# Performance work log

Hardware: AMD Instinct MI355X
Metric: run time of the kernel (lower is better)

The kernel has to match this reference:

```python
import jax, jax.numpy as jnp
import numpy as np

B, T, D, K = 4, 2048, 1024, 4

def setup_inputs() -> dict:
    key = jax.random.key(0)
    ks = jax.random.split(key, 4)
    u = jax.random.normal(ks[0], (B, T, D), dtype=jnp.float32)
    s0 = jnp.zeros((B, K, D), dtype=jnp.float32)
    W_in = jax.random.normal(ks[1], (K * D, D), dtype=jnp.float32) * (1.0 / np.sqrt(D))
    b_in = jnp.zeros((K * D,), dtype=jnp.float32)
    W_out = jax.random.normal(ks[2], (D, K * D), dtype=jnp.float32) * (1.0 / np.sqrt(K * D))
    b_out = jnp.zeros((D,), dtype=jnp.float32)
    decay_logit = jax.random.normal(ks[3], (K,), dtype=jnp.float32)
    return {"u": u, "s0": s0, "W_in": W_in, "b_in": b_in,
            "W_out": W_out, "b_out": b_out, "decay_logit": decay_logit}

def reference(u, s0, W_in, b_in, W_out, b_out, decay_logit):
    # u: (B,T,D); s0: (B,K,D)
    Bb, Tt, Dd = u.shape
    Kk = decay_logit.shape[0]
    # input projection -> (B,T,K,D) -> (T,B,K,D) for scan over time
    inp = (jnp.einsum('btd,ed->bte', u, W_in) + b_in).reshape(Bb, Tt, Kk, Dd)
    xs = jnp.transpose(inp, (1, 0, 2, 3))  # (T,B,K,D)
    decay = jax.nn.sigmoid(decay_logit).reshape(1, Kk, 1)  # (1,K,1)

    def step(s, x):
        s_next = decay * s + x
        return s_next, s_next

    s_last, s_seq = jax.lax.scan(step, s0, xs)  # s_seq: (T,B,K,D)
    g_in = jnp.transpose(s_seq, (1, 0, 2, 3)).reshape(Bb, Tt, Kk * Dd)
    g = jnp.einsum('bte,de->btd', g_in, W_out) + b_out
    return g, s_last
```

## Files before the change

kernel.cpp:

```cpp
#include <hip/hip_runtime.h>


#define Bb 4
#define Tt 2048
#define Dd 1024
#define Kk 4
#define BT (Bb*Tt)
#define Ee (Kk*Dd)
#define NCH 32
#define LCH 64

typedef __bf16 bf16x8 __attribute__((ext_vector_type(8)));
typedef float  f32x4  __attribute__((ext_vector_type(4)));

__device__ __forceinline__ float bf2f(ushort u){
  union { unsigned int i; float f; } x; x.i = ((unsigned int)u) << 16; return x.f;
}
__device__ __forceinline__ ushort f2bf(float f){
  union { unsigned int i; float f; } x; x.f = f;
  unsigned int i = x.i;
  return (ushort)((i + 0x7FFFu + ((i >> 16) & 1u)) >> 16);
}
__device__ __forceinline__ float lo16(unsigned u){
  union { unsigned i; float f; } x; x.i = u << 16; return x.f;
}
__device__ __forceinline__ float hi16(unsigned u){
  union { unsigned i; float f; } x; x.i = u & 0xFFFF0000u; return x.f;
}
__device__ __forceinline__ float sigm(float x){ return 1.0f / (1.0f + expf(-x)); }

__global__ __launch_bounds__(256) void k_f2bf4(const float4* __restrict__ in,
                                               ushort4* __restrict__ out, int n4){
  int i = blockIdx.x * 256 + threadIdx.x;
  if (i < n4){
    float4 v = in[i];
    ushort4 o; o.x = f2bf(v.x); o.y = f2bf(v.y); o.z = f2bf(v.z); o.w = f2bf(v.w);
    out[i] = o;
  }
}

__global__ __launch_bounds__(256) void k_transpose(const float* __restrict__ in,
                                                   ushort* __restrict__ out){
  __shared__ float tile[32][33];
  int tx = threadIdx.x, ty = threadIdx.y;
  int c0 = blockIdx.x * 32, r0 = blockIdx.y * 32;
  #pragma unroll
  for (int j = 0; j < 4; ++j)
    tile[ty + j*8][tx] = in[(size_t)(r0 + ty + j*8) * Dd + c0 + tx];
  __syncthreads();
  #pragma unroll
  for (int j = 0; j < 4; ++j)
    out[(size_t)(c0 + ty + j*8) * Ee + r0 + tx] = f2bf(tile[tx][ty + j*8]);
}

__global__ __launch_bounds__(256) void gemm_nt(const ushort* __restrict__ A,
                                               const ushort* __restrict__ B,
                                               ushort* __restrict__ C,
                                               int Kred, int lda, int ldb, int ldc,
                                               long aBatch, long bBatch, long cBatch){
  __shared__ ushort As[128 * 32];
  __shared__ ushort Bs[128 * 32];
  A += (long)blockIdx.z * aBatch;
  B += (long)blockIdx.z * bBatch;
  C += (long)blockIdx.z * cBatch;
  const int tid  = threadIdx.x;
  const int lane = tid & 63;
  const int w    = tid >> 6;
  const int wr   = w >> 1, wc = w & 1;
  const int rowBase = blockIdx.x * 128;
  const int colBase = blockIdx.y * 128;

  f32x4 acc[4][4] = {};
  const int krow = (lane >> 4) * 8;
  const int rsel = lane & 15;

  for (int kk = 0; kk < Kred; kk += 32){
    __syncthreads();
    #pragma unroll
    for (int i = 0; i < 2; ++i){
      int c  = i * 256 + tid;
      int r  = c >> 2;
      int c8 = (c & 3) * 8;
      const ushort* ga = A + (size_t)(rowBase + r) * lda + kk + c8;
      const ushort* gb = B + (size_t)(colBase + r) * ldb + kk + c8;
      __builtin_amdgcn_global_load_lds((const __attribute__((address_space(1))) void*)ga,
                                       (__attribute__((address_space(3))) void*)&As[c * 8],
                                       16, 0, 0);
      __builtin_amdgcn_global_load_lds((const __attribute__((address_space(1))) void*)gb,
                                       (__attribute__((address_space(3))) void*)&Bs[c * 8],
                                       16, 0, 0);
    }
    asm volatile("s_waitcnt vmcnt(0)" ::: "memory");
    __syncthreads();

    bf16x8 Af[4], Bf[4];
    #pragma unroll
    for (int mi = 0; mi < 4; ++mi)
      Af[mi] = *(const bf16x8*)&As[(wr*64 + mi*16 + rsel) * 32 + krow];
    #pragma unroll
    for (int ni = 0; ni < 4; ++ni)
      Bf[ni] = *(const bf16x8*)&Bs[(wc*64 + ni*16 + rsel) * 32 + krow];
    #pragma unroll
    for (int mi = 0; mi < 4; ++mi)
      #pragma unroll
      for (int ni = 0; ni < 4; ++ni)
        acc[mi][ni] = __builtin_amdgcn_mfma_f32_16x16x32_bf16(Af[mi], Bf[ni], acc[mi][ni], 0, 0, 0);
  }

  #pragma unroll
  for (int mi = 0; mi < 4; ++mi){
    #pragma unroll
    for (int ni = 0; ni < 4; ++ni){
      int r0 = rowBase + wr*64 + mi*16 + (lane >> 4) * 4;
      int c0 = colBase + wc*64 + ni*16 + (lane & 15);
      #pragma unroll
      for (int q = 0; q < 4; ++q)
        C[(size_t)(r0 + q) * ldc + c0] = f2bf(acc[mi][ni][q]);
    }
  }
}

#define STAGE_OP(GB, LOFF)                                                     \
  { _Pragma("unroll")                                                          \
    for (int i_ = 0; i_ < 2; ++i_){                                            \
      int c_ = tid + i_*256;                                                   \
      int row_ = c_ >> 2;                                                      \
      int ss_ = (c_ & 3) ^ ((row_ >> 2) & 3);                                  \
      const ushort* g_ = (GB) + (size_t)row_ * 1024 + ss_ * 8;                 \
      __builtin_amdgcn_global_load_lds(                                        \
        (const __attribute__((address_space(1))) void*)g_,                     \
        (__attribute__((address_space(3))) void*)&lds[(LOFF) + c_*8],          \
        16, 0, 0);                                                             \
    } }

#define LOAD_A4(DST)                                                           \
  { _Pragma("unroll")                                                          \
    for (int mi_ = 0; mi_ < 4; ++mi_){                                         \
      int r_ = wm*64 + mi_*16 + rsel;                                          \
      int uo_ = r_*32 + kq*8;                                                  \
      uo_ ^= ((uo_ >> 7) & 3) << 3;                                            \
      DST[mi_] = *(const bf16x8*)&lds[cbase + uo_];                            \
    } }

#define LOAD_B4(DST)                                                           \
  { _Pragma("unroll")                                                          \
    for (int ni_ = 0; ni_ < 4; ++ni_){                                         \
      int r_ = wn*64 + ni_*16 + rsel;                                          \
      int uo_ = r_*32 + kq*8;                                                  \
      uo_ ^= ((uo_ >> 7) & 3) << 3;                                            \
      DST[ni_] = *(const bf16x8*)&lds[cbase + 4096 + uo_];                     \
    } }

#define XB(R) ((((R) & 3) ^ (((R) >> 2) & 3)) << 5)
#define BAR() __builtin_amdgcn_s_barrier()

__global__ __launch_bounds__(256, 4) void gemm_big(const ushort* __restrict__ A,
                                                   const ushort* __restrict__ B,
                                                   ushort* __restrict__ C,
                                                   const float* __restrict__ dlog,
                                                   float* __restrict__ carry){
  __shared__ ushort lds[16384];
  const int tid  = threadIdx.x;
  const int lane = tid & 63;
  const int w    = tid >> 6;
  const int wm   = w >> 1;
  const int wn   = w & 1;
  const int rsel = lane & 15;
  const int kq   = lane >> 4;

  int bid = blockIdx.x;
  int xcd = bid & 7, rr = bid >> 3;
  const int rowBase = ((xcd >> 1) * 16 + (rr & 15)) * 128;
  const int colBase = ((xcd & 1) * 16 + (rr >> 4)) * 128;

  const ushort* Ag = A + (size_t)rowBase * 1024;
  const ushort* Bg = B + (size_t)colBase * 1024;

  f32x4 acc[4][4] = {};

  STAGE_OP(Ag +  0, 0);
  STAGE_OP(Bg +  0, 4096);
  STAGE_OP(Ag + 32, 8192);
  STAGE_OP(Bg + 32, 8192 + 4096);
  asm volatile("s_waitcnt vmcnt(4)" ::: "memory");
  BAR();

  for (int t = 0; t < 32; ++t){
    const int cbase = (t & 1) * 8192;
    bf16x8 af[4], bf[4];
    LOAD_A4(af); LOAD_B4(bf);
    #pragma unroll
    for (int mi = 0; mi < 4; ++mi)
      #pragma unroll
      for (int ni = 0; ni < 4; ++ni)
        acc[mi][ni] = __builtin_amdgcn_mfma_f32_16x16x32_bf16(af[mi], bf[ni], acc[mi][ni], 0, 0, 0);
    asm volatile("s_waitcnt lgkmcnt(0)" ::: "memory");
    BAR();
    if (t < 30){
      STAGE_OP(Ag + (t+2)*32, cbase);
      STAGE_OP(Bg + (t+2)*32, cbase + 4096);
      asm volatile("s_waitcnt vmcnt(4)" ::: "memory");
    } else {
      asm volatile("s_waitcnt vmcnt(0)" ::: "memory");
    }
    BAR();
  }

  #pragma unroll
  for (int mi = 0; mi < 4; ++mi){
    #pragma unroll
    for (int j = 0; j < 4; ++j){
      #pragma unroll
      for (int q = 0; q < 4; ++q){
        int row = wm*64 + mi*16 + (lane >> 4)*4 + q;
        int col = wn*64 + j*16 + rsel;
        int byte = (row*256 + col*2) ^ XB(row);
        *(ushort*)((char*)lds + byte) = f2bf(acc[mi][j][q]);
      }
    }
  }
  __syncthreads();

  if (tid < 128){
    const int k_blk = colBase >> 10;
    const int b_blk = rowBase >> 11;
    const int ch0   = (rowBase & 2047) >> 6;
    const int d0    = colBase & 1023;
    const float p   = sigm(dlog[k_blk]);
    int cp = tid & 63, ch = tid >> 6;
    float a0 = 0.f, a1 = 0.f;
    for (int i = 0; i < 64; ++i){
      int row = ch*64 + i;
      int byte = (row*256 + cp*4) ^ XB(row);
      unsigned v = *(const unsigned*)((char*)lds + byte);
      a0 = p * a0 + lo16(v);
      a1 = p * a1 + hi16(v);
    }
    float* cdst = &carry[(size_t)((b_blk*Kk + k_blk)*NCH + ch0 + ch) * Dd + d0 + cp*2];
    cdst[0] = a0; cdst[1] = a1;
  }

  #pragma unroll
  for (int j = 0; j < 8; ++j){
    int idx = tid + j*256;
    int r = idx >> 4, c16 = idx & 15;
    int byte = (r*256 + c16*16) ^ XB(r);
    f32x4 v = *(const f32x4*)((char*)lds + byte);
    *(f32x4*)&C[(size_t)(rowBase + r) * Ee + colBase + c16*8] = v;
  }
}

__global__ __launch_bounds__(256) void k_z0(const ushort* __restrict__ Wout_bf,
                                            const float* __restrict__ s0,
                                            float* __restrict__ z0){
  int gid  = blockIdx.x * 4 + (threadIdx.x >> 6);
  int lane = threadIdx.x & 63;
  int d = gid & 1023, k = (gid >> 10) & 3, b = gid >> 12;
  const ushort* wrow = Wout_bf + (size_t)d * Ee + k * Dd;
  const float* sv   = s0 + ((size_t)(b*Kk + k) << 10);
  float s = 0.f;
  #pragma unroll
  for (int j = 0; j < 2; ++j){
    int base = lane*8 + j*512;
    uint4 wv = *(const uint4*)(wrow + base);
    float4 sa = *(const float4*)(sv + base);
    float4 sb = *(const float4*)(sv + base + 4);
    s += lo16(wv.x)*sa.x + hi16(wv.x)*sa.y + lo16(wv.y)*sa.z + hi16(wv.y)*sa.w
       + lo16(wv.z)*sb.x + hi16(wv.z)*sb.y + lo16(wv.w)*sb.z + hi16(wv.w)*sb.w;
  }
  for (int off = 32; off; off >>= 1) s += __shfl_down(s, off);
  if (lane == 0) z0[gid] = s;
}

__global__ __launch_bounds__(256) void k_cterm(const ushort* __restrict__ Wout_bf,
                                               const float* __restrict__ b_in,
                                               float* __restrict__ cterm){
  int gid  = blockIdx.x * 4 + (threadIdx.x >> 6);
  int lane = threadIdx.x & 63;
  int d = gid & 1023, k = gid >> 10;
  const ushort* wrow = Wout_bf + (size_t)d * Ee + k * Dd;
  const float* bv   = b_in + k * Dd;
  float s = 0.f;
  #pragma unroll
  for (int j = 0; j < 2; ++j){
    int base = lane*8 + j*512;
    uint4 wv = *(const uint4*)(wrow + base);
    float4 sa = *(const float4*)(bv + base);
    float4 sb = *(const float4*)(bv + base + 4);
    s += lo16(wv.x)*sa.x + hi16(wv.x)*sa.y + lo16(wv.y)*sa.z + hi16(wv.y)*sa.w
       + lo16(wv.z)*sb.x + hi16(wv.z)*sb.y + lo16(wv.w)*sb.z + hi16(wv.w)*sb.w;
  }
  for (int off = 32; off; off >>= 1) s += __shfl_down(s, off);
  if (lane == 0) cterm[gid] = s;
}

__global__ __launch_bounds__(256) void k_scanInc(const float* __restrict__ carry,
                                                 const float* __restrict__ z0,
                                                 const float* __restrict__ dlog,
                                                 float* __restrict__ incoming){
  int idx = blockIdx.x * 256 + threadIdx.x;
  int k = (idx >> 10) & 3;
  int bk = idx >> 10, d = idx & 1023;
  float p  = sigm(dlog[k]);
  float dL = powf(p, (float)LCH);
  float inc = z0[idx];
  for (int c = 0; c < NCH; ++c){
    size_t o = ((size_t)(bk * NCH + c)) * Dd + d;
    incoming[o] = inc;
    inc = dL * inc + carry[o];
  }
}

__global__ __launch_bounds__(256) void k_scanB(const ushort* __restrict__ Y,
                                               const float* __restrict__ incoming,
                                               const float* __restrict__ dlog,
                                               const float* __restrict__ b_out,
                                               const float* __restrict__ cterm,
                                               float* __restrict__ g){
  int x = blockIdx.x;
  int d = blockIdx.y * 256 + threadIdx.x;
  int c = x & 31, b = x >> 5;
  float p[4], z[4], ct[4], pw[4];
  #pragma unroll
  for (int k = 0; k < 4; ++k){
    p[k]  = sigm(dlog[k]);
    z[k]  = incoming[((size_t)(((b*Kk + k))*NCH + c)) * Dd + d];
    float omp = fmaxf(1.0f - p[k], 1e-30f);
    ct[k] = cterm[k * Dd + d] / omp;
    pw[k] = powf(p[k], (float)(c * LCH + 1));
  }
  float bo = b_out[d];
  size_t ybase = ((size_t)(b*Tt + c*LCH)) * Ee + d;
  size_t gbase = ((size_t)(b*Tt + c*LCH)) * Dd + d;
  for (int i = 0; i < LCH; ++i){
    float acc = bo;
    #pragma unroll
    for (int k = 0; k < 4; ++k){
      z[k] = p[k] * z[k] + bf2f(Y[ybase + (size_t)k * Dd]);
      acc += z[k] + ct[k] * (1.0f - pw[k]);
      pw[k] *= p[k];
    }
    g[gbase] = acc;
    ybase += Ee; gbase += Dd;
  }
}

__global__ __launch_bounds__(256) void k_prep(const float* __restrict__ u,
                                              const float* __restrict__ dlog,
                                              float* __restrict__ vpart,
                                              ushort* __restrict__ U_bf){
  int x = blockIdx.x;
  int d = blockIdx.y * 256 + threadIdx.x;
  int c = x & 31, b = x >> 5;
  float p[4], a[4] = {0.f, 0.f, 0.f, 0.f};
  #pragma unroll
  for (int k = 0; k < 4; ++k) p[k] = sigm(dlog[k]);
  size_t ub = ((size_t)(b*Tt + c*LCH)) * Dd + d;
  for (int i = 0; i < LCH; ++i){
    float uv = u[ub];
    U_bf[ub] = f2bf(uv);
    #pragma unroll
    for (int k = 0; k < 4; ++k) a[k] = p[k] * a[k] + uv;
    ub += Dd;
  }
  #pragma unroll
  for (int k = 0; k < 4; ++k)
    vpart[(((size_t)x) * Kk + k) * Dd + d] = a[k];
}

__global__ __launch_bounds__(256) void k_vcomb(const float* __restrict__ vpart,
                                               const float* __restrict__ dlog,
                                               float* __restrict__ vfull){
  int idx = blockIdx.x * 256 + threadIdx.x;
  int k = (idx >> 10) & 3, b = idx >> 12, d = idx & 1023;
  float p  = sigm(dlog[k]);
  float dL = powf(p, (float)LCH);
  float v = 0.f;
  for (int c = 0; c < NCH; ++c)
    v = dL * v + vpart[(((size_t)(b*NCH + c)) * Kk + k) * Dd + d];
  vfull[idx] = v;
}

__global__ __launch_bounds__(256) void k_slast(const float* __restrict__ W_in,
                                               const float* __restrict__ vfull,
                                               const float* __restrict__ s0,
                                               const float* __restrict__ b_in,
                                               const float* __restrict__ dlog,
                                               float* __restrict__ out){
  int gid  = blockIdx.x * 4 + (threadIdx.x >> 6);
  int lane = threadIdx.x & 63;
  int d = gid & 1023, k = (gid >> 10) & 3, b = gid >> 12;
  const float* wrow = W_in + (size_t)(k*Dd + d) * Dd;
  const float* vv   = vfull + ((size_t)(b*Kk + k) << 10);
  float s = 0.f;
  #pragma unroll
  for (int j = 0; j < 16; ++j) s += wrow[lane + j*64] * vv[lane + j*64];
  for (int off = 32; off; off >>= 1) s += __shfl_down(s, off);
  if (lane == 0){
    float p  = sigm(dlog[k]);
    float pT = powf(p, (float)Tt);
    float omp = 1.0f - p;
    float geo = (omp < 1e-12f) ? (float)Tt : (1.0f - pT) / omp;
    out[gid] = pT * s0[gid] + s + b_in[k*Dd + d] * geo;
  }
}

extern "C" void kernel_launch(void* const* d_in, const int* in_sizes, int n_in,
                              void* d_out, int out_size, void* d_ws, size_t ws_size,
                              hipStream_t stream){
  const float* u     = (const float*)d_in[0];
  const float* s0    = (const float*)d_in[1];
  const float* W_in  = (const float*)d_in[2];
  const float* b_in  = (const float*)d_in[3];
  const float* W_out = (const float*)d_in[4];
  const float* b_out = (const float*)d_in[5];
  const float* dlog  = (const float*)d_in[6];

  float* g_out     = (float*)d_out;
  float* slast_out = g_out + (size_t)BT * Dd;

  char* ws = (char*)d_ws;
  if (ws_size < 115490816ull) return;
  ushort* U_bf    = (ushort*)(ws);
  ushort* WinT    = (ushort*)(ws + 16777216);
  ushort* Wout_bf = (ushort*)(ws + 25165824);
  ushort* Mcat    = (ushort*)(ws + 33554432);
  ushort* Y       = (ushort*)(ws + 41943040);
  float*  carry   = (float*)(ws + 109051904);
  float*  incoming= (float*)(ws + 111149056);
  float*  z0buf   = (float*)(ws + 113246208);
  float*  cterm   = (float*)(ws + 113311744);
  float*  vpart   = (float*)(ws + 113328128);
  float*  vfull   = (float*)(ws + 115425280);

  k_prep<<<dim3(128, 4), 256, 0, stream>>>(u, dlog, vpart, U_bf);
  k_f2bf4<<<4096, 256, 0, stream>>>((const float4*)W_out, (ushort4*)Wout_bf, Dd*Ee/4);
  k_transpose<<<dim3(32, 128), dim3(32, 8), 0, stream>>>(W_in, WinT);

  gemm_nt<<<dim3(8, 8, 4), 256, 0, stream>>>(Wout_bf, WinT, Mcat,
                                             1024, Ee, Ee, Dd,
                                             1024L, 1024L, 1048576L);
  gemm_big<<<2048, 256, 0, stream>>>(U_bf, Mcat, Y, dlog, carry);

  k_z0<<<4096, 256, 0, stream>>>(Wout_bf, s0, z0buf);
  k_cterm<<<1024, 256, 0, stream>>>(Wout_bf, b_in, cterm);

  k_scanInc<<<64, 256, 0, stream>>>(carry, z0buf, dlog, incoming);
  k_scanB<<<dim3(128, 4), 256, 0, stream>>>(Y, incoming, dlog, b_out, cterm, g_out);

  k_vcomb<<<64, 256, 0, stream>>>(vpart, dlog, vfull);
  k_slast<<<4096, 256, 0, stream>>>(W_in, vfull, s0, b_in, dlog, slast_out);
}
```

Baseline: 173.7 us.

## Fuse W_out bf16 conversion with z0 and cterm reductions; retune LDS swizzle

Replaces the separate W_out fp32-to-bf16 conversion, z0 and cterm kernels with a single kernel. It converts each W_out row segment and, in the same pass, reduces it against s0 for all batches and against b_in, so W_out is read once instead of three times. This also removes two launches. The reductions now use fp32 weights instead of bf16, which changes rounding slightly. Separately, the gemm_big LDS XOR swizzle is changed to key on different row bits, meant to reduce bank conflicts in the fragment reads.

```diff
diff --git a/kernel.cpp b/kernel.cpp
--- a/kernel.cpp
+++ b/kernel.cpp
@@ -29,16 +29,6 @@
 }
 __device__ __forceinline__ float sigm(float x){ return 1.0f / (1.0f + expf(-x)); }
 
-__global__ __launch_bounds__(256) void k_f2bf4(const float4* __restrict__ in,
-                                               ushort4* __restrict__ out, int n4){
-  int i = blockIdx.x * 256 + threadIdx.x;
-  if (i < n4){
-    float4 v = in[i];
-    ushort4 o; o.x = f2bf(v.x); o.y = f2bf(v.y); o.z = f2bf(v.z); o.w = f2bf(v.w);
-    out[i] = o;
-  }
-}
-
 __global__ __launch_bounds__(256) void k_transpose(const float* __restrict__ in,
                                                    ushort* __restrict__ out){
   __shared__ float tile[32][33];
@@ -51,6 +41,52 @@
   #pragma unroll
   for (int j = 0; j < 4; ++j)
     out[(size_t)(c0 + ty + j*8) * Ee + r0 + tx] = f2bf(tile[tx][ty + j*8]);
+}
+
+__global__ __launch_bounds__(256) void k_wout(const float* __restrict__ Wout,
+                                              const float* __restrict__ s0,
+                                              const float* __restrict__ b_in,
+                                              ushort* __restrict__ Wout_bf,
+                                              float* __restrict__ z0,
+                                              float* __restrict__ cterm){
+  int gid  = blockIdx.x * 4 + (threadIdx.x >> 6);
+  int lane = threadIdx.x & 63;
+  int d = gid & 1023, k = gid >> 10;
+  const float* wrow = Wout + (size_t)d * Ee + k * Dd;
+  ushort*      wbf  = Wout_bf + (size_t)d * Ee + k * Dd;
+  const float* bv   = b_in + k * Dd;
+  float sc = 0.f, sz0 = 0.f, sz1 = 0.f, sz2 = 0.f, sz3 = 0.f;
+  #pragma unroll
+  for (int j = 0; j < 4; ++j){
+    int base = lane*4 + j*256;
+    float4 wv = *(const float4*)(wrow + base);
+    ushort4 ob; ob.x = f2bf(wv.x); ob.y = f2bf(wv.y); ob.z = f2bf(wv.z); ob.w = f2bf(wv.w);
+    *(ushort4*)(wbf + base) = ob;
+    float4 bb = *(const float4*)(bv + base);
+    sc += wv.x*bb.x + wv.y*bb.y + wv.z*bb.z + wv.w*bb.w;
+    #pragma unroll
+    for (int b = 0; b < 4; ++b){
+      const float* sv = s0 + ((size_t)(b*Kk + k) << 10) + base;
+      float4 s4 = *(const float4*)sv;
+      float acc = wv.x*s4.x + wv.y*s4.y + wv.z*s4.z + wv.w*s4.w;
+      if (b == 0) sz0 += acc; else if (b == 1) sz1 += acc;
+      else if (b == 2) sz2 += acc; else sz3 += acc;
+    }
+  }
+  for (int off = 32; off; off >>= 1){
+    sc  += __shfl_down(sc, off);
+    sz0 += __shfl_down(sz0, off);
+    sz1 += __shfl_down(sz1, off);
+    sz2 += __shfl_down(sz2, off);
+    sz3 += __shfl_down(sz3, off);
+  }
+  if (lane == 0){
+    cterm[gid] = sc;
+    z0[gid]          = sz0;
+    z0[gid + 4096]   = sz1;
+    z0[gid + 8192]   = sz2;
+    z0[gid + 12288]  = sz3;
+  }
 }
 
 __global__ __launch_bounds__(256) void gemm_nt(const ushort* __restrict__ A,
@@ -125,7 +161,7 @@
     for (int i_ = 0; i_ < 2; ++i_){                                            \
       int c_ = tid + i_*256;                                                   \
       int row_ = c_ >> 2;                                                      \
-      int ss_ = (c_ & 3) ^ ((row_ >> 2) & 3);                                  \
+      int ss_ = (c_ & 3) ^ ((row_ >> 1) & 3);                                  \
       const ushort* g_ = (GB) + (size_t)row_ * 1024 + ss_ * 8;                 \
       __builtin_amdgcn_global_load_lds(                                        \
         (const __attribute__((address_space(1))) void*)g_,                     \
@@ -138,7 +174,7 @@
     for (int mi_ = 0; mi_ < 4; ++mi_){                                         \
       int r_ = wm*64 + mi_*16 + rsel;                                          \
       int uo_ = r_*32 + kq*8;                                                  \
-      uo_ ^= ((uo_ >> 7) & 3) << 3;                                            \
+      uo_ ^= ((uo_ >> 6) & 3) << 3;                                            \
       DST[mi_] = *(const bf16x8*)&lds[cbase + uo_];                            \
     } }
 
@@ -147,7 +183,7 @@
     for (int ni_ = 0; ni_ < 4; ++ni_){                                         \
       int r_ = wn*64 + ni_*16 + rsel;                                          \
       int uo_ = r_*32 + kq*8;                                                  \
-      uo_ ^= ((uo_ >> 7) & 3) << 3;                                            \
+      uo_ ^= ((uo_ >> 6) & 3) << 3;                                            \
       DST[ni_] = *(const bf16x8*)&lds[cbase + 4096 + uo_];                     \
     } }
 
@@ -250,50 +286,6 @@
   }
 }
 
-__global__ __launch_bounds__(256) void k_z0(const ushort* __restrict__ Wout_bf,
-                                            const float* __restrict__ s0,
-                                            float* __restrict__ z0){
-  int gid  = blockIdx.x * 4 + (threadIdx.x >> 6);
-  int lane = threadIdx.x & 63;
-  int d = gid & 1023, k = (gid >> 10) & 3, b = gid >> 12;
-  const ushort* wrow = Wout_bf + (size_t)d * Ee + k * Dd;
-  const float* sv   = s0 + ((size_t)(b*Kk + k) << 10);
-  float s = 0.f;
-  #pragma unroll
-  for (int j = 0; j < 2; ++j){
-    int base = lane*8 + j*512;
-    uint4 wv = *(const uint4*)(wrow + base);
-    float4 sa = *(const float4*)(sv + base);
-    float4 sb = *(const float4*)(sv + base + 4);
-    s += lo16(wv.x)*sa.x + hi16(wv.x)*sa.y + lo16(wv.y)*sa.z + hi16(wv.y)*sa.w
-       + lo16(wv.z)*sb.x + hi16(wv.z)*sb.y + lo16(wv.w)*sb.z + hi16(wv.w)*sb.w;
-  }
-  for (int off = 32; off; off >>= 1) s += __shfl_down(s, off);
-  if (lane == 0) z0[gid] = s;
-}
-
-__global__ __launch_bounds__(256) void k_cterm(const ushort* __restrict__ Wout_bf,
-                                               const float* __restrict__ b_in,
-                                               float* __restrict__ cterm){
-  int gid  = blockIdx.x * 4 + (threadIdx.x >> 6);
-  int lane = threadIdx.x & 63;
-  int d = gid & 1023, k = gid >> 10;
-  const ushort* wrow = Wout_bf + (size_t)d * Ee + k * Dd;
-  const float* bv   = b_in + k * Dd;
-  float s = 0.f;
-  #pragma unroll
-  for (int j = 0; j < 2; ++j){
-    int base = lane*8 + j*512;
-    uint4 wv = *(const uint4*)(wrow + base);
-    float4 sa = *(const float4*)(bv + base);
-    float4 sb = *(const float4*)(bv + base + 4);
-    s += lo16(wv.x)*sa.x + hi16(wv.x)*sa.y + lo16(wv.y)*sa.z + hi16(wv.y)*sa.w
-       + lo16(wv.z)*sb.x + hi16(wv.z)*sb.y + lo16(wv.w)*sb.z + hi16(wv.w)*sb.w;
-  }
-  for (int off = 32; off; off >>= 1) s += __shfl_down(s, off);
-  if (lane == 0) cterm[gid] = s;
-}
-
 __global__ __launch_bounds__(256) void k_scanInc(const float* __restrict__ carry,
                                                  const float* __restrict__ z0,
                                                  const float* __restrict__ dlog,
@@ -434,7 +426,7 @@
   float*  vfull   = (float*)(ws + 115425280);
 
   k_prep<<<dim3(128, 4), 256, 0, stream>>>(u, dlog, vpart, U_bf);
-  k_f2bf4<<<4096, 256, 0, stream>>>((const float4*)W_out, (ushort4*)Wout_bf, Dd*Ee/4);
+  k_wout<<<1024, 256, 0, stream>>>(W_out, s0, b_in, Wout_bf, z0buf, cterm);
   k_transpose<<<dim3(32, 128), dim3(32, 8), 0, stream>>>(W_in, WinT);
 
   gemm_nt<<<dim3(8, 8, 4), 256, 0, stream>>>(Wout_bf, WinT, Mcat,
@@ -442,9 +434,6 @@
                                              1024L, 1024L, 1048576L);
   gemm_big<<<2048, 256, 0, stream>>>(U_bf, Mcat, Y, dlog, carry);
 
-  k_z0<<<4096, 256, 0, stream>>>(Wout_bf, s0, z0buf);
-  k_cterm<<<1024, 256, 0, stream>>>(Wout_bf, b_in, cterm);
-
   k_scanInc<<<64, 256, 0, stream>>>(carry, z0buf, dlog, incoming);
   k_scanB<<<dim3(128, 4), 256, 0, stream>>>(Y, incoming, dlog, b_out, cterm, g_out);
 
```

New measurement: 167.3 us. 3.7% less time.
